# Performance work log

Hardware: AMD Instinct MI355X
Metric: run time of the kernel (lower is better)

Reference implementation:

```python
import jax, jax.numpy as jnp
import numpy as np

B, L, S, DE, D = 16, 2048, 1024, 512, 256
VOP, NSIL, A, NN = 64, 8, 64, 100000


def setup_inputs() -> dict:
    key = jax.random.key(0)
    ks = jax.random.split(key, 11)
    return {
        "encoded_sentence_tokens": jax.random.normal(ks[0], (B, S, DE), jnp.float32),
        "encoded_stack_nodes": jax.random.normal(ks[1], (NN, D), jnp.float32),
        "silent_embeddings": jax.random.normal(ks[2], (NSIL, D), jnp.float32),
        "op_embedding": jax.random.normal(ks[3], (VOP, D), jnp.float32) * 0.02,
        "w_shift": jax.random.normal(ks[4], (DE, D), jnp.float32) / np.sqrt(DE).astype(np.float32),
        "b_shift": jnp.zeros((D,), jnp.float32),
        "op_tokens": jax.random.randint(ks[5], (B, L), 0, VOP),
        "arg_idx": jax.random.randint(ks[6], (B, L), 0, NSIL + A),
        "shift_idx": jax.random.randint(ks[7], (B, L), 0, S),
        "item_type": jax.random.randint(ks[8], (B, L), 0, 3),
        "avail_nodes": jax.random.randint(ks[9], (B, L, A), 0, NN),
    }


def reference(encoded_sentence_tokens, encoded_stack_nodes, silent_embeddings,
              op_embedding, w_shift, b_shift,
              op_tokens, arg_idx, shift_idx, item_type, avail_nodes):
    # Operation embeddings: [B, L, D]
    emb_ops = op_embedding[op_tokens]

    # Shift-arg embeddings: gather sentence encodings per (b, l), then linear. [B, L, D]
    gathered_sent = jnp.take_along_axis(
        encoded_sentence_tokens, shift_idx[:, :, None], axis=1)  # [B, L, DE]
    emb_shift = jnp.einsum('ble,ed->bld', gathered_sent, w_shift) + b_shift

    # Argument embeddings: choice index < NSIL -> silent embedding, else stack node.
    # Equivalent to concat([silent, available_node_embs], axis=2)[arg_idx] without
    # materializing the [B, L, NSIL+A, D] choice tensor.
    is_silent = arg_idx < NSIL                                    # [B, L]
    silent_sel = silent_embeddings[jnp.clip(arg_idx, 0, NSIL - 1)]  # [B, L, D]
    node_pos = jnp.clip(arg_idx - NSIL, 0, A - 1)                 # [B, L]
    node_ids = jnp.take_along_axis(avail_nodes, node_pos[:, :, None], axis=2)[..., 0]
    node_sel = encoded_stack_nodes[node_ids]                      # [B, L, D]
    emb_args = jnp.where(is_silent[:, :, None], silent_sel, node_sel)

    # combine_embeddings: positional masks align, so it's a 3-way select by type.
    t = item_type[:, :, None]
    result = jnp.where(t == 0, emb_ops,
             jnp.where(t == 1, emb_args,
             jnp.where(t == 2, emb_shift, jnp.zeros_like(emb_ops))))
    return result
```

## Files before the change

kernel.cpp:

```cpp
#include <hip/hip_runtime.h>

#define B_    16
#define L_    2048
#define S_    1024
#define DE_   512
#define D_    256
#define NSIL_ 8
#define A_    64
#define MS_   (B_ * S_)

#define BM 64
#define BN 256
#define BK 64
#define NGEMM (MS_ / BM)
#define NT01  128

typedef __attribute__((ext_vector_type(8))) short  short8;
typedef __attribute__((ext_vector_type(4))) float  f32x4;

__device__ __forceinline__ unsigned short f2bf(float f) {
    unsigned int x = __builtin_bit_cast(unsigned int, f);
    x += 0x7fffu + ((x >> 16) & 1u);
    return (unsigned short)(x >> 16);
}
__device__ __forceinline__ float bf2f(unsigned short u) {
    unsigned int x = ((unsigned int)u) << 16;
    return __builtin_bit_cast(float, x);
}

__global__ __launch_bounds__(256) void srse_wt(
    const float* __restrict__ w, unsigned short* __restrict__ wT)
{
    __shared__ float tile[64][65];
    const int t  = threadIdx.x;
    const int kb = (blockIdx.x >> 2) << 6;
    const int nb = (blockIdx.x & 3) << 6;

    #pragma unroll
    for (int p = 0; p < 4; ++p) {
        const int id = p * 256 + t;
        const int k  = id >> 4;
        const int n4 = id & 15;
        const float4 v = *(const float4*)(w + (size_t)(kb + k) * D_ + nb + n4 * 4);
        tile[k][n4 * 4 + 0] = v.x;
        tile[k][n4 * 4 + 1] = v.y;
        tile[k][n4 * 4 + 2] = v.z;
        tile[k][n4 * 4 + 3] = v.w;
    }
    __syncthreads();

    const int n  = t >> 2;
    const int kq = t & 3;
    short8 o0, o1;
    #pragma unroll
    for (int j = 0; j < 8; ++j) o0[j] = (short)f2bf(tile[kq * 16 + j][n]);
    #pragma unroll
    for (int j = 0; j < 8; ++j) o1[j] = (short)f2bf(tile[kq * 16 + 8 + j][n]);
    *(short8*)(wT + (size_t)(nb + n) * DE_ + kb + kq * 16)     = o0;
    *(short8*)(wT + (size_t)(nb + n) * DE_ + kb + kq * 16 + 8) = o1;
}

__global__ __launch_bounds__(512) void srse_gemm_t01(
    const float*          __restrict__ sent,
    const unsigned short* __restrict__ wT,
    const float*          __restrict__ bsh,
    unsigned short*       __restrict__ Pb,
    const float*          __restrict__ op_emb,
    const float*          __restrict__ silent,
    const float*          __restrict__ nodes,
    const int*            __restrict__ op_tokens,
    const int*            __restrict__ arg_idx,
    const int*            __restrict__ item_type,
    const int*            __restrict__ avail,
    float*                __restrict__ out)
{
    __shared__ alignas(16) unsigned short As[BM * BK];
    __shared__ alignas(16) unsigned short Bs[BN * BK];

    const int t    = threadIdx.x;
    const int lane = t & 63;
    const int wid  = t >> 6;

    if (blockIdx.x < NGEMM) {
        const int gm0 = blockIdx.x * BM;
        const int wm  = wid & 1;
        const int wn  = wid >> 1;
        const int fr  = lane & 15;
        const int fq  = lane >> 4;

        f32x4 acc[2][4] = {};

        for (int k0 = 0; k0 < DE_; k0 += BK) {
            {
                const int row = t >> 3;
                const int k8  = t & 7;
                const float4 a0 = *(const float4*)(sent + (size_t)(gm0 + row) * DE_ + k0 + k8 * 8);
                const float4 a1 = *(const float4*)(sent + (size_t)(gm0 + row) * DE_ + k0 + k8 * 8 + 4);
                short8 v;
                v[0] = f2bf(a0.x); v[1] = f2bf(a0.y); v[2] = f2bf(a0.z); v[3] = f2bf(a0.w);
                v[4] = f2bf(a1.x); v[5] = f2bf(a1.y); v[6] = f2bf(a1.z); v[7] = f2bf(a1.w);
                *(short8*)(As + ((row * BK + k8 * 8) ^ ((row & 7) << 3))) = v;
            }
            #pragma unroll
            for (int p = 0; p < 4; ++p) {
                const int id = p * 512 + t;
                const int n  = id >> 3;
                const int k8 = id & 7;
                short8 v = *(const short8*)(wT + (size_t)n * DE_ + k0 + k8 * 8);
                *(short8*)(Bs + ((n * BK + k8 * 8) ^ ((n & 7) << 3))) = v;
            }
            __syncthreads();

            #pragma unroll
            for (int ks = 0; ks < 2; ++ks) {
                short8 af[2], bfr[4];
                #pragma unroll
                for (int mf = 0; mf < 2; ++mf) {
                    const int row = wm * 32 + mf * 16 + fr;
                    af[mf] = *(const short8*)(As + ((row * BK + ks * 32 + fq * 8) ^ ((row & 7) << 3)));
                }
                #pragma unroll
                for (int nf = 0; nf < 4; ++nf) {
                    const int n = wn * 64 + nf * 16 + fr;
                    bfr[nf] = *(const short8*)(Bs + ((n * BK + ks * 32 + fq * 8) ^ ((n & 7) << 3)));
                }
                #pragma unroll
                for (int mf = 0; mf < 2; ++mf)
                    #pragma unroll
                    for (int nf = 0; nf < 4; ++nf)
                        acc[mf][nf] = __builtin_amdgcn_mfma_f32_16x16x32_bf16(
                            af[mf], bfr[nf], acc[mf][nf], 0, 0, 0);
            }
            __syncthreads();
        }

        #pragma unroll
        for (int nf = 0; nf < 4; ++nf) {
            const int col = wn * 64 + nf * 16 + fr;
            const float bval = bsh[col];
            #pragma unroll
            for (int mf = 0; mf < 2; ++mf) {
                #pragma unroll
                for (int r = 0; r < 4; ++r) {
                    const int row = gm0 + wm * 32 + mf * 16 + fq * 4 + r;
                    Pb[(size_t)row * D_ + col] = f2bf(acc[mf][nf][r] + bval);
                }
            }
        }
    } else {
        const int bid2 = blockIdx.x - NGEMM;
        const int r0w  = bid2 * 256 + wid * 32;

        #pragma unroll
        for (int b4 = 0; b4 < 4; ++b4) {
            const int r0 = r0w + b4 * 8;
            const float* src[8];
            int tt8[8];
            #pragma unroll
            for (int i = 0; i < 8; ++i) {
                const int row = r0 + i;
                const int tt  = item_type[row];
                tt8[i] = tt;
                const int a = arg_idx[row];
                int np = a - NSIL_;
                np = np < 0 ? 0 : (np > A_ - 1 ? A_ - 1 : np);
                const float* s0 = op_emb + (size_t)op_tokens[row] * D_;
                const float* s1 = (a < NSIL_)
                                  ? silent + (size_t)a * D_
                                  : nodes + (size_t)avail[(size_t)row * A_ + np] * D_;
                src[i] = (tt == 0) ? s0 : s1;
            }
            float4 v[8];
            #pragma unroll
            for (int i = 0; i < 8; ++i)
                v[i] = *(const float4*)(src[i] + lane * 4);
            #pragma unroll
            for (int i = 0; i < 8; ++i)
                if (tt8[i] != 2)
                    *(float4*)(out + (size_t)(r0 + i) * D_ + lane * 4) = v[i];
        }
    }
}

__global__ __launch_bounds__(256) void srse_t2(
    const unsigned short* __restrict__ Pb,
    const int*            __restrict__ shift_idx,
    const int*            __restrict__ item_type,
    float*                __restrict__ out)
{
    const int wid  = threadIdx.x >> 6;
    const int lane = threadIdx.x & 63;
    const int r0   = blockIdx.x * 64 + wid * 16;

    int tt[16], ss[16];
    #pragma unroll
    for (int i = 0; i < 16; ++i) tt[i] = item_type[r0 + i];
    #pragma unroll
    for (int i = 0; i < 16; ++i) ss[i] = shift_idx[r0 + i];

    #pragma unroll
    for (int i = 0; i < 16; ++i) {
        if (tt[i] == 2) {
            const int row = r0 + i;
            const int b   = row >> 11;
            const unsigned short* p = Pb + (size_t)((b << 10) + ss[i]) * D_;
            const short4 x = *(const short4*)(p + lane * 4);
            float4 o;
            o.x = bf2f((unsigned short)x.x);
            o.y = bf2f((unsigned short)x.y);
            o.z = bf2f((unsigned short)x.z);
            o.w = bf2f((unsigned short)x.w);
            *(float4*)(out + (size_t)row * D_ + lane * 4) = o;
        }
    }
}

extern "C" void kernel_launch(void* const* d_in, const int* in_sizes, int n_in,
                              void* d_out, int out_size, void* d_ws, size_t ws_size,
                              hipStream_t stream) {
    const float* sent      = (const float*)d_in[0];
    const float* nodes     = (const float*)d_in[1];
    const float* silent    = (const float*)d_in[2];
    const float* op_emb    = (const float*)d_in[3];
    const float* w         = (const float*)d_in[4];
    const float* bsh       = (const float*)d_in[5];
    const int*   op_tokens = (const int*)d_in[6];
    const int*   arg_idx   = (const int*)d_in[7];
    const int*   shift_idx = (const int*)d_in[8];
    const int*   item_type = (const int*)d_in[9];
    const int*   avail     = (const int*)d_in[10];
    float*       out       = (float*)d_out;

    unsigned short* wT = (unsigned short*)d_ws;
    unsigned short* Pb = (unsigned short*)((char*)d_ws + D_ * DE_ * 2);

    srse_wt<<<32, 256, 0, stream>>>(w, wT);

    srse_gemm_t01<<<NGEMM + NT01, 512, 0, stream>>>(
        sent, wT, bsh, Pb, op_emb, silent, nodes,
        op_tokens, arg_idx, item_type, avail, out);

    srse_t2<<<(B_ * L_) / 64, 256, 0, stream>>>(Pb, shift_idx, item_type, out);
}
```

Baseline: 218.4 us.

## Fuse shift gather into GEMM A-load and drop projected intermediate buffer

Moves the shift-index gather before the projection: each GEMM block loads gathered sentence rows directly and writes fp32 results only for type-2 rows. This removes the bf16 intermediate buffer, its write/read, and the separate scatter kernel launch. In exchange the GEMM now runs over all B*L rows instead of B*S, doubling matmul work and sentence reads, and computes rows that are discarded.

```diff
diff --git a/kernel.cpp b/kernel.cpp
--- a/kernel.cpp
+++ b/kernel.cpp
@@ -7,13 +7,13 @@
 #define D_    256
 #define NSIL_ 8
 #define A_    64
-#define MS_   (B_ * S_)
+#define NR_   (B_ * L_)
 
 #define BM 64
 #define BN 256
 #define BK 64
-#define NGEMM (MS_ / BM)
-#define NT01  128
+#define NGEMM (NR_ / BM)
+#define NT01  256
 
 typedef __attribute__((ext_vector_type(8))) short  short8;
 typedef __attribute__((ext_vector_type(4))) float  f32x4;
@@ -22,10 +22,6 @@
     unsigned int x = __builtin_bit_cast(unsigned int, f);
     x += 0x7fffu + ((x >> 16) & 1u);
     return (unsigned short)(x >> 16);
-}
-__device__ __forceinline__ float bf2f(unsigned short u) {
-    unsigned int x = ((unsigned int)u) << 16;
-    return __builtin_bit_cast(float, x);
 }
 
 __global__ __launch_bounds__(256) void srse_wt(
@@ -60,16 +56,16 @@
     *(short8*)(wT + (size_t)(nb + n) * DE_ + kb + kq * 16 + 8) = o1;
 }
 
-__global__ __launch_bounds__(512) void srse_gemm_t01(
+__global__ __launch_bounds__(512) void srse_mega(
     const float*          __restrict__ sent,
     const unsigned short* __restrict__ wT,
     const float*          __restrict__ bsh,
-    unsigned short*       __restrict__ Pb,
     const float*          __restrict__ op_emb,
     const float*          __restrict__ silent,
     const float*          __restrict__ nodes,
     const int*            __restrict__ op_tokens,
     const int*            __restrict__ arg_idx,
+    const int*            __restrict__ shift_idx,
     const int*            __restrict__ item_type,
     const int*            __restrict__ avail,
     float*                __restrict__ out)
@@ -83,31 +79,37 @@
 
     if (blockIdx.x < NGEMM) {
         const int gm0 = blockIdx.x * BM;
-        const int wm  = wid & 1;
-        const int wn  = wid >> 1;
-        const int fr  = lane & 15;
-        const int fq  = lane >> 4;
+
+        const int srow = t >> 3;
+        const int k8   = t & 7;
+        const int orow = gm0 + srow;
+        const int sb   = orow >> 11;
+        const float* abase = sent + ((size_t)((sb << 10) + shift_idx[orow]) * DE_) + k8 * 8;
+        const int awidx = ((srow * BK + k8 * 8) ^ ((srow & 7) << 3));
+
+        const int wm = wid & 1;
+        const int wn = wid >> 1;
+        const int fr = lane & 15;
+        const int fq = lane >> 4;
 
         f32x4 acc[2][4] = {};
 
         for (int k0 = 0; k0 < DE_; k0 += BK) {
             {
-                const int row = t >> 3;
-                const int k8  = t & 7;
-                const float4 a0 = *(const float4*)(sent + (size_t)(gm0 + row) * DE_ + k0 + k8 * 8);
-                const float4 a1 = *(const float4*)(sent + (size_t)(gm0 + row) * DE_ + k0 + k8 * 8 + 4);
+                const float4 a0 = *(const float4*)(abase + k0);
+                const float4 a1 = *(const float4*)(abase + k0 + 4);
                 short8 v;
                 v[0] = f2bf(a0.x); v[1] = f2bf(a0.y); v[2] = f2bf(a0.z); v[3] = f2bf(a0.w);
                 v[4] = f2bf(a1.x); v[5] = f2bf(a1.y); v[6] = f2bf(a1.z); v[7] = f2bf(a1.w);
-                *(short8*)(As + ((row * BK + k8 * 8) ^ ((row & 7) << 3))) = v;
+                *(short8*)(As + awidx) = v;
             }
             #pragma unroll
             for (int p = 0; p < 4; ++p) {
                 const int id = p * 512 + t;
                 const int n  = id >> 3;
-                const int k8 = id & 7;
-                short8 v = *(const short8*)(wT + (size_t)n * DE_ + k0 + k8 * 8);
-                *(short8*)(Bs + ((n * BK + k8 * 8) ^ ((n & 7) << 3))) = v;
+                const int kb8 = id & 7;
+                short8 v = *(const short8*)(wT + (size_t)n * DE_ + k0 + kb8 * 8);
+                *(short8*)(Bs + ((n * BK + kb8 * 8) ^ ((n & 7) << 3))) = v;
             }
             __syncthreads();
 
@@ -134,6 +136,13 @@
             __syncthreads();
         }
 
+        int t2m[2][4];
+        #pragma unroll
+        for (int mf = 0; mf < 2; ++mf)
+            #pragma unroll
+            for (int r = 0; r < 4; ++r)
+                t2m[mf][r] = item_type[gm0 + wm * 32 + mf * 16 + fq * 4 + r];
+
         #pragma unroll
         for (int nf = 0; nf < 4; ++nf) {
             const int col = wn * 64 + nf * 16 + fr;
@@ -142,18 +151,20 @@
             for (int mf = 0; mf < 2; ++mf) {
                 #pragma unroll
                 for (int r = 0; r < 4; ++r) {
-                    const int row = gm0 + wm * 32 + mf * 16 + fq * 4 + r;
-                    Pb[(size_t)row * D_ + col] = f2bf(acc[mf][nf][r] + bval);
+                    if (t2m[mf][r] == 2) {
+                        const int row = gm0 + wm * 32 + mf * 16 + fq * 4 + r;
+                        out[(size_t)row * D_ + col] = acc[mf][nf][r] + bval;
+                    }
                 }
             }
         }
     } else {
         const int bid2 = blockIdx.x - NGEMM;
-        const int r0w  = bid2 * 256 + wid * 32;
+        const int r0w  = bid2 * 128 + wid * 16;
 
         #pragma unroll
-        for (int b4 = 0; b4 < 4; ++b4) {
-            const int r0 = r0w + b4 * 8;
+        for (int b8 = 0; b8 < 2; ++b8) {
+            const int r0 = r0w + b8 * 8;
             const float* src[8];
             int tt8[8];
             #pragma unroll
@@ -178,39 +189,6 @@
             for (int i = 0; i < 8; ++i)
                 if (tt8[i] != 2)
                     *(float4*)(out + (size_t)(r0 + i) * D_ + lane * 4) = v[i];
-        }
-    }
-}
-
-__global__ __launch_bounds__(256) void srse_t2(
-    const unsigned short* __restrict__ Pb,
-    const int*            __restrict__ shift_idx,
-    const int*            __restrict__ item_type,
-    float*                __restrict__ out)
-{
-    const int wid  = threadIdx.x >> 6;
-    const int lane = threadIdx.x & 63;
-    const int r0   = blockIdx.x * 64 + wid * 16;
-
-    int tt[16], ss[16];
-    #pragma unroll
-    for (int i = 0; i < 16; ++i) tt[i] = item_type[r0 + i];
-    #pragma unroll
-    for (int i = 0; i < 16; ++i) ss[i] = shift_idx[r0 + i];
-
-    #pragma unroll
-    for (int i = 0; i < 16; ++i) {
-        if (tt[i] == 2) {
-            const int row = r0 + i;
-            const int b   = row >> 11;
-            const unsigned short* p = Pb + (size_t)((b << 10) + ss[i]) * D_;
-            const short4 x = *(const short4*)(p + lane * 4);
-            float4 o;
-            o.x = bf2f((unsigned short)x.x);
-            o.y = bf2f((unsigned short)x.y);
-            o.z = bf2f((unsigned short)x.z);
-            o.w = bf2f((unsigned short)x.w);
-            *(float4*)(out + (size_t)row * D_ + lane * 4) = o;
         }
     }
 }
@@ -232,13 +210,10 @@
     float*       out       = (float*)d_out;
 
     unsigned short* wT = (unsigned short*)d_ws;
-    unsigned short* Pb = (unsigned short*)((char*)d_ws + D_ * DE_ * 2);
 
     srse_wt<<<32, 256, 0, stream>>>(w, wT);
 
-    srse_gemm_t01<<<NGEMM + NT01, 512, 0, stream>>>(
-        sent, wT, bsh, Pb, op_emb, silent, nodes,
-        op_tokens, arg_idx, item_type, avail, out);
-
-    srse_t2<<<(B_ * L_) / 64, 256, 0, stream>>>(Pb, shift_idx, item_type, out);
-}
+    srse_mega<<<NGEMM + NT01, 512, 0, stream>>>(
+        sent, wT, bsh, op_emb, silent, nodes,
+        op_tokens, arg_idx, shift_idx, item_type, avail, out);
+}
```

After: 210.7 us. -3.5%, faster.
